# Kernel tuning notes

Hardware: AMD Instinct MI355X
Metric: run time of the kernel (lower is better)

The kernel has to match this reference:

```python
import jax, jax.numpy as jnp
import numpy as np

EPS = 1e-5
HID = 32
FUSED = 33 * 33 * 33  # 35937


def _subnet(x, gamma, beta, W1, b1, W2, b2, W3, b3):
    # BatchNorm1d in training mode: batch mean / biased variance
    mu = jnp.mean(x, axis=0)
    var = jnp.mean((x - mu) ** 2, axis=0)
    xn = (x - mu) / jnp.sqrt(var + EPS) * gamma + beta
    h = jax.nn.relu(xn @ W1 + b1)
    h = jax.nn.relu(h @ W2 + b2)
    return jax.nn.relu(h @ W3 + b3)


def _subnet_params(key, in_dim):
    ks = jax.random.split(key, 6)
    s_in = 1.0 / np.sqrt(in_dim)
    s_h = 1.0 / np.sqrt(HID)
    return dict(
        gamma=jnp.ones((in_dim,), jnp.float32),
        beta=jnp.zeros((in_dim,), jnp.float32),
        W1=jax.random.uniform(ks[0], (in_dim, HID), jnp.float32, -s_in, s_in),
        b1=jax.random.uniform(ks[1], (HID,), jnp.float32, -s_in, s_in),
        W2=jax.random.uniform(ks[2], (HID, HID), jnp.float32, -s_h, s_h),
        b2=jax.random.uniform(ks[3], (HID,), jnp.float32, -s_h, s_h),
        W3=jax.random.uniform(ks[4], (HID, HID), jnp.float32, -s_h, s_h),
        b3=jax.random.uniform(ks[5], (HID,), jnp.float32, -s_h, s_h),
    )


def setup_inputs() -> dict:
    key = jax.random.key(0)
    ks = jax.random.split(key, 10)
    B = 8192
    inp = {
        'US_x': jax.random.normal(ks[0], (B, 1024), jnp.float32),
        'CDFI_x': jax.random.normal(ks[1], (B, 1024), jnp.float32),
        'marker_x': jax.random.normal(ks[2], (B, 10), jnp.float32),
    }
    for pref, k, d in (('us', ks[3], 1024), ('cd', ks[4], 1024), ('mk', ks[5], 10)):
        for n, v in _subnet_params(k, d).items():
            inp[f'{pref}_{n}'] = v
    s1 = 1.0 / np.sqrt(FUSED)
    s2 = 1.0 / np.sqrt(33)
    inp['Wf1'] = jax.random.uniform(ks[6], (FUSED, 33), jnp.float32, -s1, s1)
    inp['bf1'] = jax.random.uniform(ks[7], (33,), jnp.float32, -s1, s1)
    inp['Wf2'] = jax.random.uniform(ks[8], (33, 5), jnp.float32, -s2, s2)
    inp['bf2'] = jax.random.uniform(ks[9], (5,), jnp.float32, -s2, s2)
    return inp


def reference(US_x, CDFI_x, marker_x,
              us_gamma, us_beta, us_W1, us_b1, us_W2, us_b2, us_W3, us_b3,
              cd_gamma, cd_beta, cd_W1, cd_b1, cd_W2, cd_b2, cd_W3, cd_b3,
              mk_gamma, mk_beta, mk_W1, mk_b1, mk_W2, mk_b2, mk_W3, mk_b3,
              Wf1, bf1, Wf2, bf2):
    B = US_x.shape[0]
    us_h = _subnet(US_x, us_gamma, us_beta, us_W1, us_b1, us_W2, us_b2, us_W3, us_b3)
    cd_h = _subnet(CDFI_x, cd_gamma, cd_beta, cd_W1, cd_b1, cd_W2, cd_b2, cd_W3, cd_b3)
    mk_h = _subnet(marker_x, mk_gamma, mk_beta, mk_W1, mk_b1, mk_W2, mk_b2, mk_W3, mk_b3)
    ones = jnp.ones((B, 1), jnp.float32)
    us1 = jnp.concatenate([ones, us_h], axis=1)   # [B,33]
    cd1 = jnp.concatenate([ones, cd_h], axis=1)   # [B,33]
    mk1 = jnp.concatenate([ones, mk_h], axis=1)   # [B,33]
    # fused[b,k,j,i] = mk1[b,k] * cd1[b,j] * us1[b,i]; flattened row-major
    fused = jnp.einsum('bk,bj,bi->bkji', mk1, cd1, us1).reshape(B, FUSED)
    h = jax.nn.relu(fused @ Wf1 + bf1)
    return jax.nn.sigmoid(h @ Wf2 + bf2)
```

## Files before the change

kernel.cpp:

```cpp
#include <hip/hip_runtime.h>
#include <hip/hip_bf16.h>
#include <math.h>

typedef __hip_bfloat16 bf16;
typedef __attribute__((ext_vector_type(4))) float f32x4;
typedef __attribute__((ext_vector_type(8))) short s16x8;

#define NB 8192
#define KP 1152
#define NP 1152

struct SubP {
    const float* x; const float* gamma; const float* beta;
    const float* W1; const float* b1; const float* W2; const float* b2;
    const float* W3; const float* b3;
    float* sum; float* sumsq; float* a; float* b1p; float* hout;
    int F;
};
struct SubP3 { SubP s[3]; };

__global__ void __launch_bounds__(256) stats3_kernel(SubP3 P) {
    const SubP p = P.s[blockIdx.z];
    int t = threadIdx.x;
    int row0 = blockIdx.x * 64;
    if (p.F == 1024) {
        f32x4 s = {0.f, 0.f, 0.f, 0.f}, s2 = {0.f, 0.f, 0.f, 0.f};
        const float* xp = p.x + (size_t)row0 * 1024 + t * 4;
        #pragma unroll 8
        for (int r = 0; r < 64; r++) {
            f32x4 v = *(const f32x4*)(xp + (size_t)r * 1024);
            s += v; s2 += v * v;
        }
        int f = t * 4;
        #pragma unroll
        for (int e = 0; e < 4; e++) {
            atomicAdd(&p.sum[f + e], s[e]);
            atomicAdd(&p.sumsq[f + e], s2[e]);
        }
    } else {
        __shared__ float ls[16], ls2[16];
        if (t < 16) { ls[t] = 0.f; ls2[t] = 0.f; }
        __syncthreads();
        int F = p.F;
        for (int idx = t; idx < 64 * F; idx += 256) {
            float v = p.x[(size_t)row0 * F + idx];
            int f = idx % 10;
            atomicAdd(&ls[f], v);
            atomicAdd(&ls2[f], v * v);
        }
        __syncthreads();
        if (t < F) { atomicAdd(&p.sum[t], ls[t]); atomicAdd(&p.sumsq[t], ls2[t]); }
    }
}

__global__ void prep3_kernel(SubP3 P) {
    const SubP p = P.s[blockIdx.y];
    int f0 = blockIdx.x * 32;
    if (f0 >= p.F) return;
    int t = threadIdx.x;
    __shared__ float c_sh[32];
    __shared__ float red[8][33];
    int fc = p.F - f0; if (fc > 32) fc = 32;
    if (t < 32) {
        float c = 0.f;
        if (t < fc) {
            int f = f0 + t;
            float mu  = p.sum[f]   * (1.f / 8192.f);
            float var = p.sumsq[f] * (1.f / 8192.f) - mu * mu;
            float a = p.gamma[f] * rsqrtf(var + 1e-5f);
            p.a[f] = a;
            c = p.beta[f] - mu * a;
        }
        c_sh[t] = c;
    }
    __syncthreads();
    int h = t & 31, g = t >> 5;
    float s = 0.f;
    for (int fi = g; fi < fc; fi += 8)
        s += c_sh[fi] * p.W1[(size_t)(f0 + fi) * 32 + h];
    red[g][h] = s;
    __syncthreads();
    if (t < 32) {
        float tot = 0.f;
        #pragma unroll
        for (int gg = 0; gg < 8; gg++) tot += red[gg][t];
        atomicAdd(&p.b1p[t], tot);
    }
}

__global__ void __launch_bounds__(256) subnet3_kernel(SubP3 P) {
    const SubP p = P.s[blockIdx.y];
    const int F = p.F;
    __shared__ float smem[8832];
    float* Red = smem;
    float* H1  = smem + 3456;
    float* W23 = smem + 4608;
    float* H2  = smem;

    int t = threadIdx.x;
    int row0 = blockIdx.x * 32;
    int kg = t >> 6;
    int lane = t & 63;
    int hg = lane & 7, h0 = hg * 4;
    int rg = (lane >> 3) & 3;
    int ks = lane >> 5;

    float acc[4][8] = {};

    if (F == 1024) {
        float* Xt = smem;
        float* Wt = smem + 4224;
        int xr = t >> 3, xc = (t & 7) * 16;
        int wk = t >> 1, wh = (t & 1) * 16;
        const float* xbase = p.x + (size_t)row0 * 1024;
        f32x4 xp[4], wp[4]; float av;
        #pragma unroll
        for (int i = 0; i < 4; i++) xp[i] = *(const f32x4*)&xbase[(size_t)xr * 1024 + xc + i * 4];
        #pragma unroll
        for (int i = 0; i < 4; i++) wp[i] = *(const f32x4*)&p.W1[(size_t)wk * 32 + wh + i * 4];
        av = p.a[wk];
        int kb = (kg * 2 + ks) * 16;
        for (int c = 0; c < 8; c++) {
            __syncthreads();
            #pragma unroll
            for (int i = 0; i < 4; i++) *(f32x4*)&Xt[xr * 132 + xc + i * 4] = xp[i];
            #pragma unroll
            for (int i = 0; i < 4; i++) *(f32x4*)&Wt[wk * 36 + wh + i * 4] = wp[i] * av;
            if (c < 7) {
                int k0 = (c + 1) * 128;
                #pragma unroll
                for (int i = 0; i < 4; i++) xp[i] = *(const f32x4*)&xbase[(size_t)xr * 1024 + k0 + xc + i * 4];
                #pragma unroll
                for (int i = 0; i < 4; i++) wp[i] = *(const f32x4*)&p.W1[(size_t)(k0 + wk) * 32 + wh + i * 4];
                av = p.a[k0 + wk];
            }
            __syncthreads();
            #pragma unroll
            for (int s = 0; s < 4; s++) {
                int kk = kb + s * 4;
                f32x4 wv[4], xv[8];
                #pragma unroll
                for (int j = 0; j < 4; j++)  wv[j]  = *(const f32x4*)&Wt[(kk + j) * 36 + h0];
                #pragma unroll
                for (int ri = 0; ri < 8; ri++) xv[ri] = *(const f32x4*)&Xt[(rg + 4 * ri) * 132 + kk];
                #pragma unroll
                for (int j = 0; j < 4; j++)
                    #pragma unroll
                    for (int hi = 0; hi < 4; hi++) {
                        float w = wv[j][hi];
                        #pragma unroll
                        for (int ri = 0; ri < 8; ri++)
                            acc[hi][ri] = fmaf(w, xv[ri][j], acc[hi][ri]);
                    }
            }
        }
    } else {
        float* Xt = smem;
        float* Wt = smem + 2176;
        int kbase = (kg * 2 + ks) * 8;
        for (int k0 = 0; k0 < F; k0 += 64) {
            int kc = F - k0; if (kc > 64) kc = 64;
            int kcp = (kc + 3) & ~3;
            __syncthreads();
            for (int idx = t; idx < 32 * kcp; idx += 256) {
                int r = idx / kcp, kk = idx - r * kcp;
                Xt[r * 68 + kk] = (kk < kc) ? p.x[(size_t)(row0 + r) * F + k0 + kk] : 0.f;
            }
            for (int idx = t; idx < kcp * 32; idx += 256) {
                int kk = idx >> 5, hh = idx & 31;
                Wt[kk * 36 + hh] = (kk < kc) ? p.a[k0 + kk] * p.W1[(size_t)(k0 + kk) * 32 + hh] : 0.f;
            }
            __syncthreads();
            #pragma unroll
            for (int s = 0; s < 2; s++) {
                int kk = kbase + s * 4;
                if (kk < kcp) {
                    f32x4 wv[4], xv[8];
                    #pragma unroll
                    for (int j = 0; j < 4; j++)  wv[j]  = *(const f32x4*)&Wt[(kk + j) * 36 + h0];
                    #pragma unroll
                    for (int ri = 0; ri < 8; ri++) xv[ri] = *(const f32x4*)&Xt[(rg + 4 * ri) * 68 + kk];
                    #pragma unroll
                    for (int j = 0; j < 4; j++)
                        #pragma unroll
                        for (int hi = 0; hi < 4; hi++) {
                            float w = wv[j][hi];
                            #pragma unroll
                            for (int ri = 0; ri < 8; ri++)
                                acc[hi][ri] = fmaf(w, xv[ri][j], acc[hi][ri]);
                        }
                }
            }
        }
    }
    #pragma unroll
    for (int hi = 0; hi < 4; hi++)
        #pragma unroll
        for (int ri = 0; ri < 8; ri++)
            acc[hi][ri] += __shfl_xor(acc[hi][ri], 32);
    __syncthreads();
    if (kg > 0 && ks == 0) {
        #pragma unroll
        for (int ri = 0; ri < 8; ri++) {
            int r = rg + 4 * ri;
            f32x4 v = {acc[0][ri], acc[1][ri], acc[2][ri], acc[3][ri]};
            *(f32x4*)&Red[(kg - 1) * 1152 + r * 36 + h0] = v;
        }
    }
    for (int idx = t; idx < 1024; idx += 256) W23[(idx >> 5) * 33 + (idx & 31)] = p.W2[idx];
    __syncthreads();
    if (kg == 0 && ks == 0) {
        f32x4 b;
        #pragma unroll
        for (int hi = 0; hi < 4; hi++) b[hi] = p.b1[h0 + hi] + p.b1p[h0 + hi];
        #pragma unroll
        for (int ri = 0; ri < 8; ri++) {
            int r = rg + 4 * ri;
            f32x4 v = {acc[0][ri], acc[1][ri], acc[2][ri], acc[3][ri]};
            #pragma unroll
            for (int pp = 0; pp < 3; pp++)
                v += *(const f32x4*)&Red[pp * 1152 + r * 36 + h0];
            v += b;
            #pragma unroll
            for (int hi = 0; hi < 4; hi++)
                H1[r * 36 + h0 + hi] = fmaxf(v[hi], 0.f);
        }
    }
    __syncthreads();
    int h = t & 31, rq = t >> 5;
    {
        float a2[4] = {};
        for (int q = 0; q < 32; q++) {
            float w = W23[q * 33 + h];
            #pragma unroll
            for (int i = 0; i < 4; i++) a2[i] += H1[(rq * 4 + i) * 36 + q] * w;
        }
        float bv = p.b2[h];
        #pragma unroll
        for (int i = 0; i < 4; i++) H2[(rq * 4 + i) * 36 + h] = fmaxf(a2[i] + bv, 0.f);
    }
    __syncthreads();
    for (int idx = t; idx < 1024; idx += 256) W23[(idx >> 5) * 33 + (idx & 31)] = p.W3[idx];
    __syncthreads();
    {
        float a3[4] = {};
        for (int q = 0; q < 32; q++) {
            float w = W23[q * 33 + h];
            #pragma unroll
            for (int i = 0; i < 4; i++) a3[i] += H2[(rq * 4 + i) * 36 + q] * w;
        }
        float bv = p.b3[h];
        #pragma unroll
        for (int i = 0; i < 4; i++)
            p.hout[(size_t)(row0 + rq * 4 + i) * 32 + h] = fmaxf(a3[i] + bv, 0.f);
    }
}

__global__ void build_both(const float* __restrict__ mk_h, const float* __restrict__ us_h,
                           bf16* __restrict__ p1,
                           const float* __restrict__ Wf1, bf16* __restrict__ W2t) {
    int blk = blockIdx.x;
    int t = threadIdx.x;
    if (blk < NB) {
        int b = blk;
        __shared__ float mk1[33], us1[33];
        if (t == 0) { mk1[0] = 1.f; us1[0] = 1.f; }
        if (t < 32) mk1[t + 1] = mk_h[(size_t)b * 32 + t];
        else if (t < 64) us1[t - 31] = us_h[(size_t)b * 32 + (t - 32)];
        __syncthreads();
        if (t < 144) {
            int base = t * 8;
            s16x8 v;
            #pragma unroll
            for (int e = 0; e < 8; e++) {
                int idx = base + e;
                float val = 0.f;
                if (idx < 1089) {
                    int k = idx / 33, i = idx - k * 33;
                    val = mk1[k] * us1[i];
                }
                __hip_bfloat16 hb = __float2bfloat16(val);
                v[e] = *(short*)&hb;
            }
            *(s16x8*)(p1 + (size_t)b * KP + base) = v;
        }
    } else {
        int kj = blk - NB;
        int k = kj / 33, j = kj - k * 33;
        __shared__ float tile[1089];
        const float* src = Wf1 + (size_t)k * 35937 + (size_t)j * 1089;
        for (int idx = t; idx < 1089; idx += 192) tile[idx] = src[idx];
        __syncthreads();
        for (int idx = t; idx < 1089; idx += 192) {
            int o = idx / 33, i = idx - o * 33;
            W2t[(size_t)(j * 33 + o) * KP + k * 33 + i] = __float2bfloat16(tile[i * 33 + o]);
        }
        if (k == 0) {
            bf16 z = __float2bfloat16(0.f);
            for (int idx = t; idx < 33 * 63; idx += 192) {
                int o = idx / 63, kkp = 1089 + idx - o * 63;
                W2t[(size_t)(j * 33 + o) * KP + kkp] = z;
            }
        }
    }
}

__global__ void __launch_bounds__(256) gemm_kernel(const bf16* __restrict__ A,
                                                   const bf16* __restrict__ Bt,
                                                   bf16* __restrict__ S) {
    __shared__ __align__(16) bf16 As[128 * 64];
    __shared__ __align__(16) bf16 Bs[128 * 64];
    int t = threadIdx.x;
    int m0 = blockIdx.x * 128;
    int n0 = blockIdx.y * 128;
    int wave = t >> 6, lane = t & 63;
    int wm = (wave & 1) * 64, wn = (wave >> 1) * 64;
    int fr = lane & 15;
    int kgi = lane >> 4;

    int srow = lane >> 3;
    int sc = (lane & 7) ^ srow;
    const bf16* Ag = A  + (size_t)(m0 + srow) * KP + sc * 8;
    const bf16* Bg = Bt + (size_t)(n0 + srow) * KP + sc * 8;

    f32x4 acc[4][4] = {};

    for (int k0 = 0; k0 < KP; k0 += 64) {
        __syncthreads();
        #pragma unroll
        for (int i = 0; i < 4; i++) {
            int base = wave * 32 + i * 8;
            __builtin_amdgcn_global_load_lds(
                (const __attribute__((address_space(1))) void*)(Ag + (size_t)base * KP + k0),
                (__attribute__((address_space(3))) void*)(As + base * 64), 16, 0, 0);
        }
        #pragma unroll
        for (int i = 0; i < 4; i++) {
            int base = wave * 32 + i * 8;
            __builtin_amdgcn_global_load_lds(
                (const __attribute__((address_space(1))) void*)(Bg + (size_t)base * KP + k0),
                (__attribute__((address_space(3))) void*)(Bs + base * 64), 16, 0, 0);
        }
        __syncthreads();
        #pragma unroll
        for (int h = 0; h < 2; h++) {
            int c = h * 4 + kgi;
            int pofs = (c ^ (fr & 7)) * 8;
            s16x8 bfr[4];
            #pragma unroll
            for (int nt = 0; nt < 4; nt++)
                bfr[nt] = *(const s16x8*)(Bs + (wn + nt * 16 + fr) * 64 + pofs);
            #pragma unroll
            for (int mt = 0; mt < 4; mt++) {
                s16x8 af = *(const s16x8*)(As + (wm + mt * 16 + fr) * 64 + pofs);
                #pragma unroll
                for (int nt = 0; nt < 4; nt++)
                    acc[mt][nt] = __builtin_amdgcn_mfma_f32_16x16x32_bf16(af, bfr[nt], acc[mt][nt], 0, 0, 0);
            }
        }
    }
    int col = lane & 15, rowg = (lane >> 4) * 4;
    #pragma unroll
    for (int mt = 0; mt < 4; mt++)
        #pragma unroll
        for (int nt = 0; nt < 4; nt++)
            #pragma unroll
            for (int r = 0; r < 4; r++) {
                int gr = m0 + wm + mt * 16 + rowg + r;
                int gc = n0 + wn + nt * 16 + col;
                S[(size_t)gr * NP + gc] = __float2bfloat16(acc[mt][nt][r]);
            }
}

__global__ void __launch_bounds__(256) epilogue_kernel(const bf16* __restrict__ S,
                                const float* __restrict__ cd_h,
                                const float* __restrict__ bf1, const float* __restrict__ Wf2,
                                const float* __restrict__ bf2, float* __restrict__ out) {
    int w = threadIdx.x >> 6;
    int lane = threadIdx.x & 63;
    int b = blockIdx.x * 4 + w;
    __shared__ __align__(16) unsigned short Sl[4][1152];
    __shared__ float cdsh[4][33];
    __shared__ float hsh[4][40];
    const bf16* Srow = S + (size_t)b * NP;
    #pragma unroll
    for (int pass = 0; pass < 3; pass++) {
        int idx = lane + pass * 64;
        if (idx < 144)
            *(s16x8*)&Sl[w][idx * 8] = *(const s16x8*)(Srow + idx * 8);
    }
    if (lane == 0) cdsh[w][0] = 1.f;
    if (lane < 32) cdsh[w][lane + 1] = cd_h[(size_t)b * 32 + lane];
    __syncthreads();
    if (lane < 33) {
        float acc = bf1[lane];
        #pragma unroll 3
        for (int j = 0; j < 33; j++) {
            unsigned short sv = Sl[w][j * 33 + lane];
            acc += cdsh[w][j] * __bfloat162float(*(bf16*)&sv);
        }
        hsh[w][lane] = fmaxf(acc, 0.f);
    }
    __syncthreads();
    if (lane < 5) {
        float o = bf2[lane];
        for (int q = 0; q < 33; q++) o += hsh[w][q] * Wf2[q * 5 + lane];
        out[(size_t)b * 5 + lane] = 1.f / (1.f + expf(-o));
    }
}

extern "C" void kernel_launch(void* const* d_in, const int* in_sizes, int n_in,
                              void* d_out, int out_size, void* d_ws, size_t ws_size,
                              hipStream_t stream) {
    const float* US_x     = (const float*)d_in[0];
    const float* CDFI_x   = (const float*)d_in[1];
    const float* marker_x = (const float*)d_in[2];
    const float* Wf1      = (const float*)d_in[27];
    const float* bf1      = (const float*)d_in[28];
    const float* Wf2      = (const float*)d_in[29];
    const float* bf2      = (const float*)d_in[30];
    float* out = (float*)d_out;

    char* ws = (char*)d_ws;
    size_t off = 0;
    auto alloc = [&](size_t bytes) -> void* {
        void* p = ws + off;
        off = (off + bytes + 255) & ~(size_t)255;
        return p;
    };

    float* stat_big = (float*)alloc(3 * 2176 * sizeof(float));
    float* a_buf[3], *h_buf[3];
    for (int i = 0; i < 3; i++) {
        a_buf[i] = (float*)alloc(1024 * 4);
        h_buf[i] = (float*)alloc((size_t)NB * 32 * 4);
    }
    bf16*  p1   = (bf16*)alloc((size_t)NB * KP * 2);
    bf16*  W2t  = (bf16*)alloc((size_t)NP * KP * 2);
    bf16*  S    = (bf16*)alloc((size_t)NB * NP * 2);

    SubP3 P;
    const float* xs[3] = {US_x, CDFI_x, marker_x};
    int Fs[3] = {1024, 1024, 10};
    for (int i = 0; i < 3; i++) {
        int base = 3 + i * 8;
        P.s[i].x     = xs[i];
        P.s[i].gamma = (const float*)d_in[base + 0];
        P.s[i].beta  = (const float*)d_in[base + 1];
        P.s[i].W1    = (const float*)d_in[base + 2];
        P.s[i].b1    = (const float*)d_in[base + 3];
        P.s[i].W2    = (const float*)d_in[base + 4];
        P.s[i].b2    = (const float*)d_in[base + 5];
        P.s[i].W3    = (const float*)d_in[base + 6];
        P.s[i].b3    = (const float*)d_in[base + 7];
        P.s[i].sum   = stat_big + i * 2176;
        P.s[i].sumsq = stat_big + i * 2176 + 1024;
        P.s[i].b1p   = stat_big + i * 2176 + 2048;
        P.s[i].a     = a_buf[i];
        P.s[i].hout  = h_buf[i];
        P.s[i].F     = Fs[i];
    }

    float* us_h = h_buf[0];
    float* cd_h = h_buf[1];
    float* mk_h = h_buf[2];

    hipMemsetAsync(stat_big, 0, 3 * 2176 * sizeof(float), stream);

    stats3_kernel<<<dim3(128, 1, 3), 256, 0, stream>>>(P);
    prep3_kernel<<<dim3(32, 3), 256, 0, stream>>>(P);
    subnet3_kernel<<<dim3(256, 3), 256, 0, stream>>>(P);

    build_both<<<NB + 1089, 192, 0, stream>>>(mk_h, us_h, p1, Wf1, W2t);

    gemm_kernel<<<dim3(NB / 128, NP / 128), 256, 0, stream>>>(p1, W2t, S);

    epilogue_kernel<<<NB / 4, 256, 0, stream>>>(S, cd_h, bf1, Wf2, bf2, out);
}
```

Before: 264.1 us.

## Double-buffer GEMM A tile in LDS, load B directly to registers, halve M tile

Restructures the bf16 MFMA GEMM. The M tile shrinks from 128 to 64 rows, so the grid grows to 128x9 blocks for more parallelism. Only the A tile is staged through LDS, now double-buffered so the next tile's loads overlap the current compute. B fragments are read straight from global memory into a double-buffered register array, which removes the B LDS traffic but increases register pressure and gives up B reuse through shared memory.

```diff
diff --git a/kernel.cpp b/kernel.cpp
--- a/kernel.cpp
+++ b/kernel.cpp
@@ -308,60 +308,70 @@
 __global__ void __launch_bounds__(256) gemm_kernel(const bf16* __restrict__ A,
                                                    const bf16* __restrict__ Bt,
                                                    bf16* __restrict__ S) {
-    __shared__ __align__(16) bf16 As[128 * 64];
-    __shared__ __align__(16) bf16 Bs[128 * 64];
+    __shared__ __align__(16) bf16 As[2][64 * 64];
     int t = threadIdx.x;
-    int m0 = blockIdx.x * 128;
+    int m0 = blockIdx.x * 64;
     int n0 = blockIdx.y * 128;
     int wave = t >> 6, lane = t & 63;
-    int wm = (wave & 1) * 64, wn = (wave >> 1) * 64;
+    int wm = (wave & 1) * 32, wn = (wave >> 1) * 64;
     int fr = lane & 15;
     int kgi = lane >> 4;
 
     int srow = lane >> 3;
     int sc = (lane & 7) ^ srow;
-    const bf16* Ag = A  + (size_t)(m0 + srow) * KP + sc * 8;
-    const bf16* Bg = Bt + (size_t)(n0 + srow) * KP + sc * 8;
-
-    f32x4 acc[4][4] = {};
-
-    for (int k0 = 0; k0 < KP; k0 += 64) {
-        __syncthreads();
-        #pragma unroll
-        for (int i = 0; i < 4; i++) {
-            int base = wave * 32 + i * 8;
+    const bf16* Ag = A + (size_t)(m0 + srow) * KP + sc * 8;
+    const bf16* Bg = Bt + (size_t)(n0 + wn + fr) * KP + kgi * 8;
+
+    f32x4 acc[2][4] = {};
+    s16x8 Bq[2][8];
+
+    auto stageA = [&](int it, int buf) {
+        #pragma unroll
+        for (int i = 0; i < 2; i++) {
+            int rbase = wave * 16 + i * 8;
             __builtin_amdgcn_global_load_lds(
-                (const __attribute__((address_space(1))) void*)(Ag + (size_t)base * KP + k0),
-                (__attribute__((address_space(3))) void*)(As + base * 64), 16, 0, 0);
-        }
-        #pragma unroll
-        for (int i = 0; i < 4; i++) {
-            int base = wave * 32 + i * 8;
-            __builtin_amdgcn_global_load_lds(
-                (const __attribute__((address_space(1))) void*)(Bg + (size_t)base * KP + k0),
-                (__attribute__((address_space(3))) void*)(Bs + base * 64), 16, 0, 0);
-        }
-        __syncthreads();
+                (const __attribute__((address_space(1))) void*)(Ag + (size_t)rbase * KP + it * 64),
+                (__attribute__((address_space(3))) void*)(As[buf] + rbase * 64), 16, 0, 0);
+        }
+    };
+    auto loadB = [&](int it, int buf) {
+        #pragma unroll
+        for (int nt = 0; nt < 4; nt++)
+            #pragma unroll
+            for (int h = 0; h < 2; h++)
+                Bq[buf][nt * 2 + h] = *(const s16x8*)(Bg + (size_t)(nt * 16) * KP + it * 64 + h * 32);
+    };
+    auto compute = [&](int buf) {
         #pragma unroll
         for (int h = 0; h < 2; h++) {
-            int c = h * 4 + kgi;
-            int pofs = (c ^ (fr & 7)) * 8;
-            s16x8 bfr[4];
-            #pragma unroll
-            for (int nt = 0; nt < 4; nt++)
-                bfr[nt] = *(const s16x8*)(Bs + (wn + nt * 16 + fr) * 64 + pofs);
-            #pragma unroll
-            for (int mt = 0; mt < 4; mt++) {
-                s16x8 af = *(const s16x8*)(As + (wm + mt * 16 + fr) * 64 + pofs);
+            int pofs = ((h * 4 + kgi) ^ (fr & 7)) * 8;
+            s16x8 af[2];
+            #pragma unroll
+            for (int mt = 0; mt < 2; mt++)
+                af[mt] = *(const s16x8*)(As[buf] + (wm + mt * 16 + fr) * 64 + pofs);
+            #pragma unroll
+            for (int mt = 0; mt < 2; mt++)
                 #pragma unroll
                 for (int nt = 0; nt < 4; nt++)
-                    acc[mt][nt] = __builtin_amdgcn_mfma_f32_16x16x32_bf16(af, bfr[nt], acc[mt][nt], 0, 0, 0);
-            }
-        }
-    }
+                    acc[mt][nt] = __builtin_amdgcn_mfma_f32_16x16x32_bf16(
+                        af[mt], Bq[buf][nt * 2 + h], acc[mt][nt], 0, 0, 0);
+        }
+    };
+
+    stageA(0, 0);
+    loadB(0, 0);
+    for (int it = 0; it < 18; it += 2) {
+        __syncthreads();
+        if (it + 1 < 18) { stageA(it + 1, 1); loadB(it + 1, 1); }
+        compute(0);
+        __syncthreads();
+        if (it + 2 < 18) { stageA(it + 2, 0); loadB(it + 2, 0); }
+        compute(1);
+    }
+
     int col = lane & 15, rowg = (lane >> 4) * 4;
     #pragma unroll
-    for (int mt = 0; mt < 4; mt++)
+    for (int mt = 0; mt < 2; mt++)
         #pragma unroll
         for (int nt = 0; nt < 4; nt++)
             #pragma unroll
@@ -473,7 +483,7 @@
 
     build_both<<<NB + 1089, 192, 0, stream>>>(mk_h, us_h, p1, Wf1, W2t);
 
-    gemm_kernel<<<dim3(NB / 128, NP / 128), 256, 0, stream>>>(p1, W2t, S);
+    gemm_kernel<<<dim3(128, 9), 256, 0, stream>>>(p1, W2t, S);
 
     epilogue_kernel<<<NB / 4, 256, 0, stream>>>(S, cd_h, bf1, Wf2, bf2, out);
 }
```

Result: slower. 309.6 us (+17.2%).
